# Performance work log

Measured on AMD Instinct MI355X. Metric: run time of the kernel, lower is better.

The kernel has to match this reference:

```python
import jax, jax.numpy as jnp
import numpy as np

EPS = 1e-06
K = 16  # instance ids 1..K
W_IOU, W_VAR, W_SEED = 1.0, 10.0, 1.0


def _lovasz_hinge_flat(logits, labels):
    # logits, labels: (N,) flat; labels in {0,1}
    signs = 2.0 * labels - 1.0
    errors = 1.0 - logits * signs
    perm = jnp.argsort(-errors)  # descending
    errors_sorted = errors[perm]
    gt_sorted = labels[perm]
    gts = gt_sorted.sum()
    intersection = gts - jnp.cumsum(gt_sorted)
    union = gts + jnp.cumsum(1.0 - gt_sorted)
    jaccard = 1.0 - intersection / jnp.maximum(union, 1e-08)
    jaccard = jnp.concatenate([jaccard[:1], jaccard[1:] - jaccard[:-1]])
    return jnp.dot(jax.nn.relu(errors_sorted), jaccard)


def _forward(y_pred, y_true):
    B, C, H, W = y_pred.shape
    D = 2
    off = y_pred[:, :D]              # (B,D,H,W)
    sig = y_pred[:, D:2 * D]         # (B,D,H,W)
    seed = y_pred[:, 2 * D]          # (B,H,W)
    dt = y_pred.dtype

    gy, gx = jnp.meshgrid(jnp.arange(H, dtype=dt), jnp.arange(W, dtype=dt), indexing='ij')
    grid = jnp.stack([gy, gx])       # (D,H,W)
    emb = grid[None] + off           # (B,D,H,W)

    ids = jnp.arange(1, K + 1)
    mask = (y_true[:, None] == ids[None, :, None, None]).astype(dt)  # (B,K,H,W)
    count = mask.sum((2, 3))                                         # (B,K)
    safe = jnp.maximum(count, 1.0)
    present = (count > 0).astype(dt)
    n_present = jnp.maximum(present.sum(), 1.0)

    # per-instance embedding centers
    Ck = jnp.einsum('bkhw,bdhw->bkd', mask, emb) / safe[..., None]   # (B,K,D)
    sb = jnp.maximum(sig, EPS)                                       # (B,D,H,W)
    diff = emb[:, None] - Ck[..., None, None]                        # (B,K,D,H,W)
    quad = diff * diff / (2.0 * sb[:, None] ** 2)
    phi = jnp.clip(jnp.exp(-quad.sum(2)), EPS, 1.0 - EPS)            # (B,K,H,W)
    logits = jnp.log(phi) - jnp.log1p(-phi)

    lov = jax.vmap(_lovasz_hinge_flat)(logits.reshape(B * K, -1), mask.reshape(B * K, -1))
    L_iou = (lov * present.reshape(-1)).sum() / n_present

    # sigma smoothness: mean over instances of mean_{d,pixels in mask}|sig - mean_k(sig)|
    mean_sig = jnp.einsum('bkhw,bdhw->bkd', mask, sig) / safe[..., None]  # (B,K,D)
    dev = (jnp.abs(sig[:, None] - mean_sig[..., None, None]) * mask[:, :, None]).sum((2, 3, 4))
    dev = dev / (D * safe)                                           # (B,K)
    L_var = (dev * present).sum() / n_present

    seed_target = (phi * mask).sum(1)                                # (B,H,W)
    L_seed = jnp.mean((seed - seed_target) ** 2)

    return W_IOU * L_iou + W_VAR * L_var + W_SEED * L_seed


def setup_inputs() -> dict:
    key = jax.random.key(0)
    k1, k2 = jax.random.split(key)
    B, H, W = 4, 768, 768
    y_pred = jax.random.uniform(k1, (B, 5, H, W), dtype=jnp.float32)
    y_true = jax.random.randint(k2, (B, H, W), 0, K + 1)
    return {"y_pred": y_pred, "y_true": y_true}


def reference(y_pred, y_true):
    return _forward(y_pred, y_true)
```

## Files before the change

### kernel.cpp

```cpp
#include <hip/hip_runtime.h>

#define HWPIX 589824
#define Wdim 768
#define Bdim 4
#define Kdim 16
#define NBINS 2048
#define RANGE_F 16.0f
#define BIN_W (RANGE_F / NBINS)
#define INV_BIN_W (NBINS / RANGE_F)
#define EPSf 1e-6f
#define QCLIP 13.8155106f

#define Q4 (HWPIX / 4)
#define NSB 192
#define NBLK (NSB * Bdim)
#define GPI (NSB * 256)

#define ACC_OFF 0
#define LOVARR_OFF 724
#define HIST_OFF_F 1024
#define NHIST (Bdim * Kdim * 2 * NBINS)
#define SPART_OFF (HIST_OFF_F + NHIST + 64)
#define MPART_OFF (SPART_OFF + NBLK * 80)

__global__ __launch_bounds__(256, 3) void k_stats(const float* __restrict__ yp,
                                                  const int* __restrict__ yt,
                                                  float* __restrict__ ws,
                                                  unsigned* __restrict__ hist) {
    int b = blockIdx.y;
    int lane = threadIdx.x & 63;
    int wv = threadIdx.x >> 6;
    __shared__ float lpart[4][80];

    {
        int gtid = (b * NSB + blockIdx.x) * 256 + threadIdx.x;
        for (int i = gtid; i < NHIST + 64; i += NBLK * 256) hist[i] = 0u;
    }

    const float4* bp4 = (const float4*)(yp + (size_t)b * 5 * HWPIX);
    const int4* bt4 = (const int4*)(yt + (size_t)b * HWPIX);

    float acc[80];
#pragma unroll
    for (int v = 0; v < 80; ++v) acc[v] = 0.f;

    for (int p = 0; p < 3; ++p) {
        int g = p * GPI + blockIdx.x * 256 + threadIdx.x;
        float4 voy = bp4[g];
        float4 vox = bp4[g + Q4];
        float4 vsy = bp4[g + 2 * Q4];
        float4 vsx = bp4[g + 3 * Q4];
        int4 vt = bt4[g];
        int hwb = g * 4;
        float oy[4] = {voy.x, voy.y, voy.z, voy.w};
        float ox[4] = {vox.x, vox.y, vox.z, vox.w};
        float sy[4] = {vsy.x, vsy.y, vsy.z, vsy.w};
        float sx[4] = {vsx.x, vsx.y, vsx.z, vsx.w};
        int tt[4] = {vt.x, vt.y, vt.z, vt.w};
#pragma unroll
        for (int j = 0; j < 4; ++j) {
            int hw = hwb + j;
            int h = hw / Wdim;
            int w = hw - h * Wdim;
            int own = tt[j] - 1;
            float vy = (float)h + oy[j];
            float vx = (float)w + ox[j];
#pragma unroll
            for (int k = 0; k < Kdim; ++k) {
                float m = (own == k) ? 1.0f : 0.0f;
                acc[k * 5 + 0] += m;
                acc[k * 5 + 1] = fmaf(m, vy, acc[k * 5 + 1]);
                acc[k * 5 + 2] = fmaf(m, vx, acc[k * 5 + 2]);
                acc[k * 5 + 3] = fmaf(m, sy[j], acc[k * 5 + 3]);
                acc[k * 5 + 4] = fmaf(m, sx[j], acc[k * 5 + 4]);
            }
        }
    }

    bool lo = (lane < 32);
#pragma unroll
    for (int v = 0; v < 40; ++v) {
        float send = lo ? acc[v + 40] : acc[v];
        float got = __shfl_xor(send, 32);
        acc[v] += lo ? got : 0.f;
        acc[v + 40] += lo ? 0.f : got;
    }
#pragma unroll
    for (int v = 0; v < 40; ++v) {
        float x = lo ? acc[v] : acc[v + 40];
#pragma unroll
        for (int o = 16; o >= 1; o >>= 1) x += __shfl_xor(x, o);
        if ((lane & 31) == 0) lpart[wv][lo ? v : v + 40] = x;
    }
    __syncthreads();
    if (threadIdx.x < 80) {
        float v = lpart[0][threadIdx.x] + lpart[1][threadIdx.x] +
                  lpart[2][threadIdx.x] + lpart[3][threadIdx.x];
        ws[SPART_OFF + (size_t)(b * NSB + blockIdx.x) * 80 + threadIdx.x] = v;
    }
}

__global__ void k_centers2(float* __restrict__ ws) {
    int wv = threadIdx.x >> 6;
    int lane = threadIdx.x & 63;
    int gw = blockIdx.x * 4 + wv;
    int b = gw / 80, idx = gw - b * 80;
    const float* sp = ws + SPART_OFF + (size_t)b * NSB * 80 + idx;
    float x = sp[(size_t)lane * 80] + sp[(size_t)(lane + 64) * 80] +
              sp[(size_t)(lane + 128) * 80];
#pragma unroll
    for (int o = 32; o >= 1; o >>= 1) x += __shfl_xor(x, o);
    if (lane == 0) ws[ACC_OFF + b * 80 + idx] = x;
}

__global__ __launch_bounds__(256, 3) void k_main(const float* __restrict__ yp,
                                                 const int* __restrict__ yt,
                                                 float* __restrict__ ws,
                                                 unsigned* __restrict__ hist) {
    int b = blockIdx.y;
    int lane = threadIdx.x & 63;
    int wv = threadIdx.x >> 6;
    __shared__ float ck_s[32];
    __shared__ float4 msw_s[17];
    __shared__ float part[4][2];
    if (threadIdx.x < 16) {
        int k = threadIdx.x;
        const float* a = ws + ACC_OFF + (size_t)b * 80 + k * 5;
        float cnt = a[0];
        float safe = fmaxf(cnt, 1.0f);
        float inv = 1.0f / safe;
        ck_s[k * 2 + 0] = a[1] * inv;
        ck_s[k * 2 + 1] = a[2] * inv;
        float4 mw;
        mw.x = a[3] * inv;
        mw.y = a[4] * inv;
        mw.z = (cnt > 0.f) ? 0.5f / cnt : 0.f;
        mw.w = 0.f;
        msw_s[k] = mw;
    }
    if (threadIdx.x == 16) msw_s[16] = (float4){0.f, 0.f, 0.f, 0.f};
    __syncthreads();

    float cky[Kdim], ckx[Kdim];
#pragma unroll
    for (int k = 0; k < Kdim; ++k) {
        cky[k] = ck_s[k * 2];
        ckx[k] = ck_s[k * 2 + 1];
    }

    unsigned* hb = hist + (size_t)(b * Kdim) * 2 * NBINS;
    unsigned* posnh = hist + (size_t)NHIST;
    const float4* bp4 = (const float4*)(yp + (size_t)b * 5 * HWPIX);
    const int4* bt4 = (const int4*)(yt + (size_t)b * HWPIX);

    float varsum = 0.f, ssum = 0.f;
    for (int p = 0; p < 3; ++p) {
        int g = p * GPI + blockIdx.x * 256 + threadIdx.x;
        float4 voy = bp4[g];
        float4 vox = bp4[g + Q4];
        float4 vsy = bp4[g + 2 * Q4];
        float4 vsx = bp4[g + 3 * Q4];
        float4 vse = bp4[g + 4 * Q4];
        int4 vt = bt4[g];
        int hwb = g * 4;
        float oy[4] = {voy.x, voy.y, voy.z, voy.w};
        float ox[4] = {vox.x, vox.y, vox.z, vox.w};
        float sya[4] = {vsy.x, vsy.y, vsy.z, vsy.w};
        float sxa[4] = {vsx.x, vsx.y, vsx.z, vsx.w};
        float sea[4] = {vse.x, vse.y, vse.z, vse.w};
        int tt[4] = {vt.x, vt.y, vt.z, vt.w};
#pragma unroll
        for (int j = 0; j < 4; ++j) {
            int hw = hwb + j;
            int h = hw / Wdim;
            int w = hw - h * Wdim;
            int own = tt[j] - 1;
            float sy = sya[j], sx = sxa[j];
            float ey = (float)h + oy[j], ex = (float)w + ox[j];
            float sby = fmaxf(sy, EPSf), sbx = fmaxf(sx, EPSf);
            float iy = 0.5f / (sby * sby), ix = 0.5f / (sbx * sbx);

            unsigned sm = 0;
#pragma unroll
            for (int k = 0; k < Kdim; ++k) {
                float dy = ey - cky[k];
                float dx = ex - ckx[k];
                float q = fmaf(dy * dy, iy, dx * dx * ix);
                if (q < QCLIP) sm |= (1u << k);
            }
            int ow = (own >= 0) ? own : 16;
            float4 mw = msw_s[ow];
            float devv = fabsf(sy - mw.x) + fabsf(sx - mw.y);
            varsum = fmaf(devv, mw.z, varsum);

            float st = (own >= 0) ? EPSf : 0.f;
            while (sm) {
                int k = __ffs(sm) - 1;
                sm &= sm - 1;
                float dy = ey - ck_s[k * 2];
                float dx = ex - ck_s[k * 2 + 1];
                float q = fmaf(dy * dy, iy, dx * dx * ix);
                float phi = expf(-q);
                phi = fminf(fmaxf(phi, EPSf), 1.0f - EPSf);
                float lg = logf(phi) - log1pf(-phi);
                bool isPos = (k == own);
                float e;
                if (isPos) {
                    st = phi;
                    atomicAdd(&posnh[b * Kdim + k], 1u);
                    e = 1.0f - lg;
                } else {
                    e = 1.0f + lg;
                }
                if (e > 0.f) {
                    int bin = (int)(e * INV_BIN_W);
                    if (bin > NBINS - 1) bin = NBINS - 1;
                    atomicAdd(&hb[(k * 2 + (isPos ? 1 : 0)) * NBINS + bin], 1u);
                }
            }
            float dd = sea[j] - st;
            ssum = fmaf(dd, dd, ssum);
        }
    }
#pragma unroll
    for (int o = 32; o >= 1; o >>= 1) {
        varsum += __shfl_xor(varsum, o);
        ssum += __shfl_xor(ssum, o);
    }
    if (lane == 0) {
        part[wv][0] = varsum;
        part[wv][1] = ssum;
    }
    __syncthreads();
    if (threadIdx.x < 2) {
        float v = part[0][threadIdx.x] + part[1][threadIdx.x] +
                  part[2][threadIdx.x] + part[3][threadIdx.x];
        ws[MPART_OFF + (size_t)(b * NSB + blockIdx.x) * 2 + threadIdx.x] = v;
    }
}

__global__ void k_lovasz(float* __restrict__ ws, const unsigned* __restrict__ hist) {
    int i = blockIdx.x;
    int lane = threadIdx.x;
    float P = ws[ACC_OFF + i * 5];
    if (P < 0.5f) {
        if (lane == 0) ws[LOVARR_OFF + i] = 0.f;
        return;
    }
    const unsigned* hn = hist + (size_t)i * 2 * NBINS;
    const unsigned* hp = hn + NBINS;
    const unsigned* posnh = hist + (size_t)NHIST;
    const float C_LO = logf(EPSf) - log1pf(-EPSf);
    const int HOTBIN = (int)((1.0f - C_LO) * INV_BIN_W);
    int deficit = (int)(P + 0.5f) - (int)posnh[i];
    int carry_p = 0, carry_n = 0;
    float Jtop = 0.f;
    float trap = 0.f;
    for (int c = NBINS / 64 - 1; c >= 0; --c) {
        int m = c * 64 + lane;
        int vp = (int)hp[m];
        int vn = (int)hn[m];
        if (m == HOTBIN) vp += deficit;
        for (int o = 1; o < 64; o <<= 1) {
            int tp = __shfl_down(vp, o);
            int tn = __shfl_down(vn, o);
            if (lane + o < 64) { vp += tp; vn += tn; }
        }
        float p_edge = (float)(carry_p + vp);
        float n_edge = (float)(carry_n + vn);
        float J = 1.0f - (P - p_edge) / (P + n_edge);
        float Jn = __shfl_down(J, 1);
        if (lane == 63) Jn = Jtop;
        trap += 0.5f * (J + Jn);
        carry_p += __shfl(vp, 0);
        carry_n += __shfl(vn, 0);
        Jtop = __shfl(J, 0);
    }
    for (int o = 1; o < 64; o <<= 1) {
        float t2 = __shfl_down(trap, o);
        if (lane + o < 64) trap += t2;
    }
    if (lane == 0) ws[LOVARR_OFF + i] = trap * BIN_W;
}

__global__ void k_final(const float* __restrict__ ws, float* __restrict__ out) {
    __shared__ float r0[256], r1[256], r2[256], r3[256];
    int t = threadIdx.x;
    float v = 0.f, s = 0.f, l = 0.f, pr = 0.f;
    for (int j = t; j < NBLK; j += 256) {
        v += ws[MPART_OFF + 2 * j];
        s += ws[MPART_OFF + 2 * j + 1];
    }
    if (t < 64) {
        l = ws[LOVARR_OFF + t];
        pr = (ws[ACC_OFF + t * 5] > 0.f) ? 1.f : 0.f;
    }
    r0[t] = v; r1[t] = s; r2[t] = l; r3[t] = pr;
    __syncthreads();
    for (int o = 128; o > 0; o >>= 1) {
        if (t < o) {
            r0[t] += r0[t + o]; r1[t] += r1[t + o];
            r2[t] += r2[t + o]; r3[t] += r3[t + o];
        }
        __syncthreads();
    }
    if (t == 0) {
        float npres = fmaxf(r3[0], 1.0f);
        out[0] = r2[0] / npres + 10.0f * (r0[0] / npres) +
                 r1[0] / (float)((size_t)Bdim * HWPIX);
    }
}

extern "C" void kernel_launch(void* const* d_in, const int* in_sizes, int n_in,
                              void* d_out, int out_size, void* d_ws, size_t ws_size,
                              hipStream_t stream) {
    const float* yp = (const float*)d_in[0];
    const int* yt = (const int*)d_in[1];
    float* ws = (float*)d_ws;
    unsigned* hist = (unsigned*)((char*)d_ws + HIST_OFF_F * 4);

    dim3 g(NSB, Bdim);
    k_stats<<<g, 256, 0, stream>>>(yp, yt, ws, hist);
    k_centers2<<<80, 256, 0, stream>>>(ws);
    k_main<<<g, 256, 0, stream>>>(yp, yt, ws, hist);
    k_lovasz<<<64, 64, 0, stream>>>(ws, hist);
    k_final<<<1, 256, 0, stream>>>(ws, (float*)d_out);
}
```

Measured before the change: 82.74 us.

## Raise grid to 288 blocks per image, split stats accumulators, preload both tiles

Increases blocks per image from 192 to 288 so each thread handles two float4 tiles instead of three, and raises launch_bounds occupancy from 3 to 4. k_stats now splits its 80-register accumulator into two phases (count/centers, then sigma sums) to cut register pressure. k_main issues all loads for both tiles up front to overlap memory latency. The trade-off is more partials for k_centers2 to reduce, which now uses a loop, and reloading the label tile in the second stats phase.

```diff
diff --git a/kernel.cpp b/kernel.cpp
--- a/kernel.cpp
+++ b/kernel.cpp
@@ -12,7 +12,7 @@
 #define QCLIP 13.8155106f
 
 #define Q4 (HWPIX / 4)
-#define NSB 192
+#define NSB 288
 #define NBLK (NSB * Bdim)
 #define GPI (NSB * 256)
 
@@ -23,7 +23,7 @@
 #define SPART_OFF (HIST_OFF_F + NHIST + 64)
 #define MPART_OFF (SPART_OFF + NBLK * 80)
 
-__global__ __launch_bounds__(256, 3) void k_stats(const float* __restrict__ yp,
+__global__ __launch_bounds__(256, 4) void k_stats(const float* __restrict__ yp,
                                                   const int* __restrict__ yt,
                                                   float* __restrict__ ws,
                                                   unsigned* __restrict__ hist) {
@@ -34,64 +34,118 @@
 
     {
         int gtid = (b * NSB + blockIdx.x) * 256 + threadIdx.x;
-        for (int i = gtid; i < NHIST + 64; i += NBLK * 256) hist[i] = 0u;
+        if (gtid < NHIST + 64) hist[gtid] = 0u;
     }
 
     const float4* bp4 = (const float4*)(yp + (size_t)b * 5 * HWPIX);
     const int4* bt4 = (const int4*)(yt + (size_t)b * HWPIX);
-
-    float acc[80];
-#pragma unroll
-    for (int v = 0; v < 80; ++v) acc[v] = 0.f;
-
-    for (int p = 0; p < 3; ++p) {
-        int g = p * GPI + blockIdx.x * 256 + threadIdx.x;
-        float4 voy = bp4[g];
-        float4 vox = bp4[g + Q4];
-        float4 vsy = bp4[g + 2 * Q4];
-        float4 vsx = bp4[g + 3 * Q4];
-        int4 vt = bt4[g];
-        int hwb = g * 4;
-        float oy[4] = {voy.x, voy.y, voy.z, voy.w};
-        float ox[4] = {vox.x, vox.y, vox.z, vox.w};
-        float sy[4] = {vsy.x, vsy.y, vsy.z, vsy.w};
-        float sx[4] = {vsx.x, vsx.y, vsx.z, vsx.w};
-        int tt[4] = {vt.x, vt.y, vt.z, vt.w};
-#pragma unroll
-        for (int j = 0; j < 4; ++j) {
-            int hw = hwb + j;
-            int h = hw / Wdim;
-            int w = hw - h * Wdim;
-            int own = tt[j] - 1;
-            float vy = (float)h + oy[j];
-            float vx = (float)w + ox[j];
-#pragma unroll
-            for (int k = 0; k < Kdim; ++k) {
-                float m = (own == k) ? 1.0f : 0.0f;
-                acc[k * 5 + 0] += m;
-                acc[k * 5 + 1] = fmaf(m, vy, acc[k * 5 + 1]);
-                acc[k * 5 + 2] = fmaf(m, vx, acc[k * 5 + 2]);
-                acc[k * 5 + 3] = fmaf(m, sy[j], acc[k * 5 + 3]);
-                acc[k * 5 + 4] = fmaf(m, sx[j], acc[k * 5 + 4]);
+    int g0 = blockIdx.x * 256 + threadIdx.x;
+    int g1 = g0 + GPI;
+    bool lo = (lane < 32);
+
+    {
+        float acc[48];
+#pragma unroll
+        for (int v = 0; v < 48; ++v) acc[v] = 0.f;
+
+        float4 aoy = bp4[g0], aox = bp4[g0 + Q4];
+        int4 at = bt4[g0];
+        float4 boy = bp4[g1], box = bp4[g1 + Q4];
+        int4 bt = bt4[g1];
+
+#define S1_TILE(voy, vox, vt, gbase)                                          \
+        do {                                                                  \
+            int hwb = (gbase) * 4;                                            \
+            float oy[4] = {voy.x, voy.y, voy.z, voy.w};                       \
+            float ox[4] = {vox.x, vox.y, vox.z, vox.w};                       \
+            int tt[4] = {vt.x, vt.y, vt.z, vt.w};                             \
+            _Pragma("unroll") for (int j = 0; j < 4; ++j) {                   \
+                int hw = hwb + j;                                             \
+                int h = hw / Wdim;                                            \
+                int w = hw - h * Wdim;                                        \
+                int own = tt[j] - 1;                                          \
+                float vy = (float)h + oy[j];                                  \
+                float vx = (float)w + ox[j];                                  \
+                _Pragma("unroll") for (int k = 0; k < Kdim; ++k) {            \
+                    float m = (own == k) ? 1.0f : 0.0f;                       \
+                    acc[k * 3 + 0] += m;                                      \
+                    acc[k * 3 + 1] = fmaf(m, vy, acc[k * 3 + 1]);             \
+                    acc[k * 3 + 2] = fmaf(m, vx, acc[k * 3 + 2]);             \
+                }                                                             \
+            }                                                                 \
+        } while (0)
+
+        S1_TILE(aoy, aox, at, g0);
+        S1_TILE(boy, box, bt, g1);
+#undef S1_TILE
+
+#pragma unroll
+        for (int v = 0; v < 24; ++v) {
+            float send = lo ? acc[v + 24] : acc[v];
+            float got = __shfl_xor(send, 32);
+            acc[v] += lo ? got : 0.f;
+            acc[v + 24] += lo ? 0.f : got;
+        }
+#pragma unroll
+        for (int v = 0; v < 24; ++v) {
+            float x = lo ? acc[v] : acc[v + 24];
+#pragma unroll
+            for (int o = 16; o >= 1; o >>= 1) x += __shfl_xor(x, o);
+            if ((lane & 31) == 0) {
+                int vv = lo ? v : v + 24;
+                lpart[wv][(vv / 3) * 5 + vv % 3] = x;
             }
         }
     }
 
-    bool lo = (lane < 32);
-#pragma unroll
-    for (int v = 0; v < 40; ++v) {
-        float send = lo ? acc[v + 40] : acc[v];
-        float got = __shfl_xor(send, 32);
-        acc[v] += lo ? got : 0.f;
-        acc[v + 40] += lo ? 0.f : got;
-    }
-#pragma unroll
-    for (int v = 0; v < 40; ++v) {
-        float x = lo ? acc[v] : acc[v + 40];
-#pragma unroll
-        for (int o = 16; o >= 1; o >>= 1) x += __shfl_xor(x, o);
-        if ((lane & 31) == 0) lpart[wv][lo ? v : v + 40] = x;
-    }
+    {
+        float acc[32];
+#pragma unroll
+        for (int v = 0; v < 32; ++v) acc[v] = 0.f;
+
+        float4 asy = bp4[g0 + 2 * Q4], asx = bp4[g0 + 3 * Q4];
+        int4 at = bt4[g0];
+        float4 bsy = bp4[g1 + 2 * Q4], bsx = bp4[g1 + 3 * Q4];
+        int4 bt = bt4[g1];
+
+#define S2_TILE(vsy, vsx, vt)                                                 \
+        do {                                                                  \
+            float sy[4] = {vsy.x, vsy.y, vsy.z, vsy.w};                       \
+            float sx[4] = {vsx.x, vsx.y, vsx.z, vsx.w};                       \
+            int tt[4] = {vt.x, vt.y, vt.z, vt.w};                             \
+            _Pragma("unroll") for (int j = 0; j < 4; ++j) {                   \
+                int own = tt[j] - 1;                                          \
+                _Pragma("unroll") for (int k = 0; k < Kdim; ++k) {            \
+                    float m = (own == k) ? 1.0f : 0.0f;                       \
+                    acc[k * 2 + 0] = fmaf(m, sy[j], acc[k * 2 + 0]);          \
+                    acc[k * 2 + 1] = fmaf(m, sx[j], acc[k * 2 + 1]);          \
+                }                                                             \
+            }                                                                 \
+        } while (0)
+
+        S2_TILE(asy, asx, at);
+        S2_TILE(bsy, bsx, bt);
+#undef S2_TILE
+
+#pragma unroll
+        for (int v = 0; v < 16; ++v) {
+            float send = lo ? acc[v + 16] : acc[v];
+            float got = __shfl_xor(send, 32);
+            acc[v] += lo ? got : 0.f;
+            acc[v + 16] += lo ? 0.f : got;
+        }
+#pragma unroll
+        for (int v = 0; v < 16; ++v) {
+            float x = lo ? acc[v] : acc[v + 16];
+#pragma unroll
+            for (int o = 16; o >= 1; o >>= 1) x += __shfl_xor(x, o);
+            if ((lane & 31) == 0) {
+                int vv = lo ? v : v + 16;
+                lpart[wv][(vv / 2) * 5 + 3 + (vv & 1)] = x;
+            }
+        }
+    }
+
     __syncthreads();
     if (threadIdx.x < 80) {
         float v = lpart[0][threadIdx.x] + lpart[1][threadIdx.x] +
@@ -106,14 +160,14 @@
     int gw = blockIdx.x * 4 + wv;
     int b = gw / 80, idx = gw - b * 80;
     const float* sp = ws + SPART_OFF + (size_t)b * NSB * 80 + idx;
-    float x = sp[(size_t)lane * 80] + sp[(size_t)(lane + 64) * 80] +
-              sp[(size_t)(lane + 128) * 80];
+    float x = 0.f;
+    for (int j = lane; j < NSB; j += 64) x += sp[(size_t)j * 80];
 #pragma unroll
     for (int o = 32; o >= 1; o >>= 1) x += __shfl_xor(x, o);
     if (lane == 0) ws[ACC_OFF + b * 80 + idx] = x;
 }
 
-__global__ __launch_bounds__(256, 3) void k_main(const float* __restrict__ yp,
+__global__ __launch_bounds__(256, 4) void k_main(const float* __restrict__ yp,
                                                  const int* __restrict__ yt,
                                                  float* __restrict__ ws,
                                                  unsigned* __restrict__ hist) {
@@ -152,76 +206,81 @@
     unsigned* posnh = hist + (size_t)NHIST;
     const float4* bp4 = (const float4*)(yp + (size_t)b * 5 * HWPIX);
     const int4* bt4 = (const int4*)(yt + (size_t)b * HWPIX);
+    int g0 = blockIdx.x * 256 + threadIdx.x;
+    int g1 = g0 + GPI;
+
+    float4 aoy = bp4[g0], aox = bp4[g0 + Q4], asy = bp4[g0 + 2 * Q4];
+    float4 asx = bp4[g0 + 3 * Q4], ase = bp4[g0 + 4 * Q4];
+    int4 at = bt4[g0];
+    float4 boy = bp4[g1], box = bp4[g1 + Q4], bsy = bp4[g1 + 2 * Q4];
+    float4 bsx = bp4[g1 + 3 * Q4], bse = bp4[g1 + 4 * Q4];
+    int4 btt = bt4[g1];
 
     float varsum = 0.f, ssum = 0.f;
-    for (int p = 0; p < 3; ++p) {
-        int g = p * GPI + blockIdx.x * 256 + threadIdx.x;
-        float4 voy = bp4[g];
-        float4 vox = bp4[g + Q4];
-        float4 vsy = bp4[g + 2 * Q4];
-        float4 vsx = bp4[g + 3 * Q4];
-        float4 vse = bp4[g + 4 * Q4];
-        int4 vt = bt4[g];
-        int hwb = g * 4;
-        float oy[4] = {voy.x, voy.y, voy.z, voy.w};
-        float ox[4] = {vox.x, vox.y, vox.z, vox.w};
-        float sya[4] = {vsy.x, vsy.y, vsy.z, vsy.w};
-        float sxa[4] = {vsx.x, vsx.y, vsx.z, vsx.w};
-        float sea[4] = {vse.x, vse.y, vse.z, vse.w};
-        int tt[4] = {vt.x, vt.y, vt.z, vt.w};
-#pragma unroll
-        for (int j = 0; j < 4; ++j) {
-            int hw = hwb + j;
-            int h = hw / Wdim;
-            int w = hw - h * Wdim;
-            int own = tt[j] - 1;
-            float sy = sya[j], sx = sxa[j];
-            float ey = (float)h + oy[j], ex = (float)w + ox[j];
-            float sby = fmaxf(sy, EPSf), sbx = fmaxf(sx, EPSf);
-            float iy = 0.5f / (sby * sby), ix = 0.5f / (sbx * sbx);
-
-            unsigned sm = 0;
-#pragma unroll
-            for (int k = 0; k < Kdim; ++k) {
-                float dy = ey - cky[k];
-                float dx = ex - ckx[k];
-                float q = fmaf(dy * dy, iy, dx * dx * ix);
-                if (q < QCLIP) sm |= (1u << k);
-            }
-            int ow = (own >= 0) ? own : 16;
-            float4 mw = msw_s[ow];
-            float devv = fabsf(sy - mw.x) + fabsf(sx - mw.y);
-            varsum = fmaf(devv, mw.z, varsum);
-
-            float st = (own >= 0) ? EPSf : 0.f;
-            while (sm) {
-                int k = __ffs(sm) - 1;
-                sm &= sm - 1;
-                float dy = ey - ck_s[k * 2];
-                float dx = ex - ck_s[k * 2 + 1];
-                float q = fmaf(dy * dy, iy, dx * dx * ix);
-                float phi = expf(-q);
-                phi = fminf(fmaxf(phi, EPSf), 1.0f - EPSf);
-                float lg = logf(phi) - log1pf(-phi);
-                bool isPos = (k == own);
-                float e;
-                if (isPos) {
-                    st = phi;
-                    atomicAdd(&posnh[b * Kdim + k], 1u);
-                    e = 1.0f - lg;
-                } else {
-                    e = 1.0f + lg;
-                }
-                if (e > 0.f) {
-                    int bin = (int)(e * INV_BIN_W);
-                    if (bin > NBINS - 1) bin = NBINS - 1;
-                    atomicAdd(&hb[(k * 2 + (isPos ? 1 : 0)) * NBINS + bin], 1u);
-                }
-            }
-            float dd = sea[j] - st;
-            ssum = fmaf(dd, dd, ssum);
-        }
-    }
+
+#define M_TILE(voy, vox, vsy, vsx, vse, vt, gbase)                            \
+    do {                                                                      \
+        int hwb = (gbase) * 4;                                                \
+        float oy[4] = {voy.x, voy.y, voy.z, voy.w};                           \
+        float ox[4] = {vox.x, vox.y, vox.z, vox.w};                           \
+        float sya[4] = {vsy.x, vsy.y, vsy.z, vsy.w};                          \
+        float sxa[4] = {vsx.x, vsx.y, vsx.z, vsx.w};                          \
+        float sea[4] = {vse.x, vse.y, vse.z, vse.w};                          \
+        int tt[4] = {vt.x, vt.y, vt.z, vt.w};                                 \
+        _Pragma("unroll") for (int j = 0; j < 4; ++j) {                       \
+            int hw = hwb + j;                                                 \
+            int h = hw / Wdim;                                                \
+            int w = hw - h * Wdim;                                            \
+            int own = tt[j] - 1;                                              \
+            float sy = sya[j], sx = sxa[j];                                   \
+            float ey = (float)h + oy[j], ex = (float)w + ox[j];               \
+            float sby = fmaxf(sy, EPSf), sbx = fmaxf(sx, EPSf);               \
+            float iy = 0.5f / (sby * sby), ix = 0.5f / (sbx * sbx);           \
+            unsigned sm = 0;                                                  \
+            _Pragma("unroll") for (int k = 0; k < Kdim; ++k) {                \
+                float dy = ey - cky[k];                                       \
+                float dx = ex - ckx[k];                                       \
+                float q = fmaf(dy * dy, iy, dx * dx * ix);                    \
+                if (q < QCLIP) sm |= (1u << k);                               \
+            }                                                                 \
+            int ow = (own >= 0) ? own : 16;                                   \
+            float4 mw = msw_s[ow];                                            \
+            float devv = fabsf(sy - mw.x) + fabsf(sx - mw.y);                 \
+            varsum = fmaf(devv, mw.z, varsum);                                \
+            float st = (own >= 0) ? EPSf : 0.f;                               \
+            while (sm) {                                                      \
+                int k = __ffs(sm) - 1;                                        \
+                sm &= sm - 1;                                                 \
+                float dy = ey - ck_s[k * 2];                                  \
+                float dx = ex - ck_s[k * 2 + 1];                              \
+                float q = fmaf(dy * dy, iy, dx * dx * ix);                    \
+                float phi = expf(-q);                                         \
+                phi = fminf(fmaxf(phi, EPSf), 1.0f - EPSf);                   \
+                float lg = logf(phi) - log1pf(-phi);                          \
+                bool isPos = (k == own);                                      \
+                float e;                                                      \
+                if (isPos) {                                                  \
+                    st = phi;                                                 \
+                    atomicAdd(&posnh[b * Kdim + k], 1u);                      \
+                    e = 1.0f - lg;                                            \
+                } else {                                                      \
+                    e = 1.0f + lg;                                            \
+                }                                                             \
+                if (e > 0.f) {                                                \
+                    int bin = (int)(e * INV_BIN_W);                           \
+                    if (bin > NBINS - 1) bin = NBINS - 1;                     \
+                    atomicAdd(&hb[(k * 2 + (isPos ? 1 : 0)) * NBINS + bin], 1u); \
+                }                                                             \
+            }                                                                 \
+            float dd = sea[j] - st;                                           \
+            ssum = fmaf(dd, dd, ssum);                                        \
+        }                                                                     \
+    } while (0)
+
+    M_TILE(aoy, aox, asy, asx, ase, at, g0);
+    M_TILE(boy, box, bsy, bsx, bse, btt, g1);
+#undef M_TILE
+
 #pragma unroll
     for (int o = 32; o >= 1; o >>= 1) {
         varsum += __shfl_xor(varsum, o);
```

New measurement: 286.9 us. 3.47x slower.

## Split stats kernel into embedding and sigma passes, widen grid, preload tiles

Applied to the files above, without the earlier changes.

The per-instance stats kernel is split into two kernels, one accumulating counts and embedding sums and one accumulating sigma sums, which cuts per-thread accumulator registers from 80 to 48 and 32. The grid grows from 192 to 288 blocks per batch so each thread handles two float4 groups instead of three. All global loads are issued up front before compute, and launch bounds raise the occupancy target to 4 blocks per CU. The cost is an extra kernel launch, a second read of the label array, and a hist zeroing that now relies on the larger grid covering the whole buffer in one pass.

```diff
diff --git a/kernel.cpp b/kernel.cpp
--- a/kernel.cpp
+++ b/kernel.cpp
@@ -12,7 +12,7 @@
 #define QCLIP 13.8155106f
 
 #define Q4 (HWPIX / 4)
-#define NSB 192
+#define NSB 288
 #define NBLK (NSB * Bdim)
 #define GPI (NSB * 256)
 
@@ -23,40 +23,40 @@
 #define SPART_OFF (HIST_OFF_F + NHIST + 64)
 #define MPART_OFF (SPART_OFF + NBLK * 80)
 
-__global__ __launch_bounds__(256, 3) void k_stats(const float* __restrict__ yp,
-                                                  const int* __restrict__ yt,
-                                                  float* __restrict__ ws,
-                                                  unsigned* __restrict__ hist) {
+__global__ __launch_bounds__(256, 4) void k_statsE(const float* __restrict__ yp,
+                                                   const int* __restrict__ yt,
+                                                   float* __restrict__ ws,
+                                                   unsigned* __restrict__ hist) {
     int b = blockIdx.y;
     int lane = threadIdx.x & 63;
     int wv = threadIdx.x >> 6;
-    __shared__ float lpart[4][80];
+    __shared__ float lpart[4][48];
 
     {
         int gtid = (b * NSB + blockIdx.x) * 256 + threadIdx.x;
-        for (int i = gtid; i < NHIST + 64; i += NBLK * 256) hist[i] = 0u;
+        if (gtid < NHIST + 64) hist[gtid] = 0u;
     }
 
     const float4* bp4 = (const float4*)(yp + (size_t)b * 5 * HWPIX);
     const int4* bt4 = (const int4*)(yt + (size_t)b * HWPIX);
-
-    float acc[80];
-#pragma unroll
-    for (int v = 0; v < 80; ++v) acc[v] = 0.f;
-
-    for (int p = 0; p < 3; ++p) {
-        int g = p * GPI + blockIdx.x * 256 + threadIdx.x;
-        float4 voy = bp4[g];
-        float4 vox = bp4[g + Q4];
-        float4 vsy = bp4[g + 2 * Q4];
-        float4 vsx = bp4[g + 3 * Q4];
-        int4 vt = bt4[g];
-        int hwb = g * 4;
+    int g0 = blockIdx.x * 256 + threadIdx.x;
+    int g1 = g0 + GPI;
+
+    float4 aoy = bp4[g0], aox = bp4[g0 + Q4];
+    int4 ait = bt4[g0];
+    float4 boy = bp4[g1], box = bp4[g1 + Q4];
+    int4 bit = bt4[g1];
+
+    float acc[48];
+#pragma unroll
+    for (int v = 0; v < 48; ++v) acc[v] = 0.f;
+
+    auto tile = [&](const float4& voy, const float4& vox, const int4& vt,
+                    int gbase) {
         float oy[4] = {voy.x, voy.y, voy.z, voy.w};
         float ox[4] = {vox.x, vox.y, vox.z, vox.w};
-        float sy[4] = {vsy.x, vsy.y, vsy.z, vsy.w};
-        float sx[4] = {vsx.x, vsx.y, vsx.z, vsx.w};
         int tt[4] = {vt.x, vt.y, vt.z, vt.w};
+        int hwb = gbase * 4;
 #pragma unroll
         for (int j = 0; j < 4; ++j) {
             int hw = hwb + j;
@@ -68,35 +68,100 @@
 #pragma unroll
             for (int k = 0; k < Kdim; ++k) {
                 float m = (own == k) ? 1.0f : 0.0f;
-                acc[k * 5 + 0] += m;
-                acc[k * 5 + 1] = fmaf(m, vy, acc[k * 5 + 1]);
-                acc[k * 5 + 2] = fmaf(m, vx, acc[k * 5 + 2]);
-                acc[k * 5 + 3] = fmaf(m, sy[j], acc[k * 5 + 3]);
-                acc[k * 5 + 4] = fmaf(m, sx[j], acc[k * 5 + 4]);
+                acc[k * 3 + 0] += m;
+                acc[k * 3 + 1] = fmaf(m, vy, acc[k * 3 + 1]);
+                acc[k * 3 + 2] = fmaf(m, vx, acc[k * 3 + 2]);
             }
         }
-    }
+    };
+    tile(aoy, aox, ait, g0);
+    tile(boy, box, bit, g1);
 
     bool lo = (lane < 32);
 #pragma unroll
-    for (int v = 0; v < 40; ++v) {
-        float send = lo ? acc[v + 40] : acc[v];
+    for (int v = 0; v < 24; ++v) {
+        float send = lo ? acc[v + 24] : acc[v];
         float got = __shfl_xor(send, 32);
         acc[v] += lo ? got : 0.f;
-        acc[v + 40] += lo ? 0.f : got;
-    }
-#pragma unroll
-    for (int v = 0; v < 40; ++v) {
-        float x = lo ? acc[v] : acc[v + 40];
+        acc[v + 24] += lo ? 0.f : got;
+    }
+#pragma unroll
+    for (int v = 0; v < 24; ++v) {
+        float x = lo ? acc[v] : acc[v + 24];
 #pragma unroll
         for (int o = 16; o >= 1; o >>= 1) x += __shfl_xor(x, o);
-        if ((lane & 31) == 0) lpart[wv][lo ? v : v + 40] = x;
+        if ((lane & 31) == 0) lpart[wv][lo ? v : v + 24] = x;
     }
     __syncthreads();
-    if (threadIdx.x < 80) {
+    if (threadIdx.x < 48) {
         float v = lpart[0][threadIdx.x] + lpart[1][threadIdx.x] +
                   lpart[2][threadIdx.x] + lpart[3][threadIdx.x];
-        ws[SPART_OFF + (size_t)(b * NSB + blockIdx.x) * 80 + threadIdx.x] = v;
+        int slot = (threadIdx.x / 3) * 5 + threadIdx.x % 3;
+        ws[SPART_OFF + (size_t)(b * NSB + blockIdx.x) * 80 + slot] = v;
+    }
+}
+
+__global__ __launch_bounds__(256, 4) void k_statsS(const float* __restrict__ yp,
+                                                   const int* __restrict__ yt,
+                                                   float* __restrict__ ws) {
+    int b = blockIdx.y;
+    int lane = threadIdx.x & 63;
+    int wv = threadIdx.x >> 6;
+    __shared__ float lpart[4][32];
+
+    const float4* bp4 = (const float4*)(yp + (size_t)b * 5 * HWPIX);
+    const int4* bt4 = (const int4*)(yt + (size_t)b * HWPIX);
+    int g0 = blockIdx.x * 256 + threadIdx.x;
+    int g1 = g0 + GPI;
+
+    float4 asy = bp4[g0 + 2 * Q4], asx = bp4[g0 + 3 * Q4];
+    int4 ait = bt4[g0];
+    float4 bsy = bp4[g1 + 2 * Q4], bsx = bp4[g1 + 3 * Q4];
+    int4 bit = bt4[g1];
+
+    float acc[32];
+#pragma unroll
+    for (int v = 0; v < 32; ++v) acc[v] = 0.f;
+
+    auto tile = [&](const float4& vsy, const float4& vsx, const int4& vt) {
+        float sy[4] = {vsy.x, vsy.y, vsy.z, vsy.w};
+        float sx[4] = {vsx.x, vsx.y, vsx.z, vsx.w};
+        int tt[4] = {vt.x, vt.y, vt.z, vt.w};
+#pragma unroll
+        for (int j = 0; j < 4; ++j) {
+            int own = tt[j] - 1;
+#pragma unroll
+            for (int k = 0; k < Kdim; ++k) {
+                float m = (own == k) ? 1.0f : 0.0f;
+                acc[k * 2 + 0] = fmaf(m, sy[j], acc[k * 2 + 0]);
+                acc[k * 2 + 1] = fmaf(m, sx[j], acc[k * 2 + 1]);
+            }
+        }
+    };
+    tile(asy, asx, ait);
+    tile(bsy, bsx, bit);
+
+    bool lo = (lane < 32);
+#pragma unroll
+    for (int v = 0; v < 16; ++v) {
+        float send = lo ? acc[v + 16] : acc[v];
+        float got = __shfl_xor(send, 32);
+        acc[v] += lo ? got : 0.f;
+        acc[v + 16] += lo ? 0.f : got;
+    }
+#pragma unroll
+    for (int v = 0; v < 16; ++v) {
+        float x = lo ? acc[v] : acc[v + 16];
+#pragma unroll
+        for (int o = 16; o >= 1; o >>= 1) x += __shfl_xor(x, o);
+        if ((lane & 31) == 0) lpart[wv][lo ? v : v + 16] = x;
+    }
+    __syncthreads();
+    if (threadIdx.x < 32) {
+        float v = lpart[0][threadIdx.x] + lpart[1][threadIdx.x] +
+                  lpart[2][threadIdx.x] + lpart[3][threadIdx.x];
+        int slot = (threadIdx.x / 2) * 5 + 3 + (threadIdx.x & 1);
+        ws[SPART_OFF + (size_t)(b * NSB + blockIdx.x) * 80 + slot] = v;
     }
 }
 
@@ -106,14 +171,14 @@
     int gw = blockIdx.x * 4 + wv;
     int b = gw / 80, idx = gw - b * 80;
     const float* sp = ws + SPART_OFF + (size_t)b * NSB * 80 + idx;
-    float x = sp[(size_t)lane * 80] + sp[(size_t)(lane + 64) * 80] +
-              sp[(size_t)(lane + 128) * 80];
+    float x = 0.f;
+    for (int j = lane; j < NSB; j += 64) x += sp[(size_t)j * 80];
 #pragma unroll
     for (int o = 32; o >= 1; o >>= 1) x += __shfl_xor(x, o);
     if (lane == 0) ws[ACC_OFF + b * 80 + idx] = x;
 }
 
-__global__ __launch_bounds__(256, 3) void k_main(const float* __restrict__ yp,
+__global__ __launch_bounds__(256, 4) void k_main(const float* __restrict__ yp,
                                                  const int* __restrict__ yt,
                                                  float* __restrict__ ws,
                                                  unsigned* __restrict__ hist) {
@@ -152,23 +217,28 @@
     unsigned* posnh = hist + (size_t)NHIST;
     const float4* bp4 = (const float4*)(yp + (size_t)b * 5 * HWPIX);
     const int4* bt4 = (const int4*)(yt + (size_t)b * HWPIX);
+    int g0 = blockIdx.x * 256 + threadIdx.x;
+    int g1 = g0 + GPI;
+
+    float4 aoy = bp4[g0], aox = bp4[g0 + Q4], asy = bp4[g0 + 2 * Q4];
+    float4 asx = bp4[g0 + 3 * Q4], ase = bp4[g0 + 4 * Q4];
+    int4 ait = bt4[g0];
+    float4 boy = bp4[g1], box = bp4[g1 + Q4], bsy = bp4[g1 + 2 * Q4];
+    float4 bsx = bp4[g1 + 3 * Q4], bse = bp4[g1 + 4 * Q4];
+    int4 bit = bt4[g1];
 
     float varsum = 0.f, ssum = 0.f;
-    for (int p = 0; p < 3; ++p) {
-        int g = p * GPI + blockIdx.x * 256 + threadIdx.x;
-        float4 voy = bp4[g];
-        float4 vox = bp4[g + Q4];
-        float4 vsy = bp4[g + 2 * Q4];
-        float4 vsx = bp4[g + 3 * Q4];
-        float4 vse = bp4[g + 4 * Q4];
-        int4 vt = bt4[g];
-        int hwb = g * 4;
+
+    auto tile = [&](const float4& voy, const float4& vox, const float4& vsy,
+                    const float4& vsx, const float4& vse, const int4& vt,
+                    int gbase) {
         float oy[4] = {voy.x, voy.y, voy.z, voy.w};
         float ox[4] = {vox.x, vox.y, vox.z, vox.w};
         float sya[4] = {vsy.x, vsy.y, vsy.z, vsy.w};
         float sxa[4] = {vsx.x, vsx.y, vsx.z, vsx.w};
         float sea[4] = {vse.x, vse.y, vse.z, vse.w};
         int tt[4] = {vt.x, vt.y, vt.z, vt.w};
+        int hwb = gbase * 4;
 #pragma unroll
         for (int j = 0; j < 4; ++j) {
             int hw = hwb + j;
@@ -221,7 +291,10 @@
             float dd = sea[j] - st;
             ssum = fmaf(dd, dd, ssum);
         }
-    }
+    };
+    tile(aoy, aox, asy, asx, ase, ait, g0);
+    tile(boy, box, bsy, bsx, bse, bit, g1);
+
 #pragma unroll
     for (int o = 32; o >= 1; o >>= 1) {
         varsum += __shfl_xor(varsum, o);
@@ -320,7 +393,8 @@
     unsigned* hist = (unsigned*)((char*)d_ws + HIST_OFF_F * 4);
 
     dim3 g(NSB, Bdim);
-    k_stats<<<g, 256, 0, stream>>>(yp, yt, ws, hist);
+    k_statsE<<<g, 256, 0, stream>>>(yp, yt, ws, hist);
+    k_statsS<<<g, 256, 0, stream>>>(yp, yt, ws);
     k_centers2<<<80, 256, 0, stream>>>(ws);
     k_main<<<g, 256, 0, stream>>>(yp, yt, ws, hist);
     k_lovasz<<<64, 64, 0, stream>>>(ws, hist);
```

New measurement: 117.1 us. 1.42x slower.

## Prefetch next pixel group in stats/main loops and fuse final reduction into lovasz

Applied to the files above, without the earlier changes.

Both pixel-streaming kernels now load the next group's float4 inputs before computing on the current group, a software-pipelined double buffer meant to hide global memory latency. The separate k_final launch is removed. The last k_lovasz block, chosen by an atomic ticket counter placed in the zeroed histogram tail, performs the final reduction, which saves one kernel launch. The risks are higher register pressure under launch_bounds(256,3) and reliance on threadfence ordering for the last-block pattern.

```diff
diff --git a/kernel.cpp b/kernel.cpp
--- a/kernel.cpp
+++ b/kernel.cpp
@@ -20,7 +20,8 @@
 #define LOVARR_OFF 724
 #define HIST_OFF_F 1024
 #define NHIST (Bdim * Kdim * 2 * NBINS)
-#define SPART_OFF (HIST_OFF_F + NHIST + 64)
+#define HTAIL 80
+#define SPART_OFF (HIST_OFF_F + NHIST + 128)
 #define MPART_OFF (SPART_OFF + NBLK * 80)
 
 __global__ __launch_bounds__(256, 3) void k_stats(const float* __restrict__ yp,
@@ -34,7 +35,7 @@
 
     {
         int gtid = (b * NSB + blockIdx.x) * 256 + threadIdx.x;
-        for (int i = gtid; i < NHIST + 64; i += NBLK * 256) hist[i] = 0u;
+        for (int i = gtid; i < NHIST + HTAIL; i += NBLK * 256) hist[i] = 0u;
     }
 
     const float4* bp4 = (const float4*)(yp + (size_t)b * 5 * HWPIX);
@@ -44,36 +45,52 @@
 #pragma unroll
     for (int v = 0; v < 80; ++v) acc[v] = 0.f;
 
+    int g = blockIdx.x * 256 + threadIdx.x;
+    float4 coy = bp4[g], cox = bp4[g + Q4];
+    float4 csy = bp4[g + 2 * Q4], csx = bp4[g + 3 * Q4];
+    int4 ct = bt4[g];
+
+#pragma unroll
     for (int p = 0; p < 3; ++p) {
-        int g = p * GPI + blockIdx.x * 256 + threadIdx.x;
-        float4 voy = bp4[g];
-        float4 vox = bp4[g + Q4];
-        float4 vsy = bp4[g + 2 * Q4];
-        float4 vsx = bp4[g + 3 * Q4];
-        int4 vt = bt4[g];
-        int hwb = g * 4;
-        float oy[4] = {voy.x, voy.y, voy.z, voy.w};
-        float ox[4] = {vox.x, vox.y, vox.z, vox.w};
-        float sy[4] = {vsy.x, vsy.y, vsy.z, vsy.w};
-        float sx[4] = {vsx.x, vsx.y, vsx.z, vsx.w};
-        int tt[4] = {vt.x, vt.y, vt.z, vt.w};
-#pragma unroll
-        for (int j = 0; j < 4; ++j) {
-            int hw = hwb + j;
-            int h = hw / Wdim;
-            int w = hw - h * Wdim;
-            int own = tt[j] - 1;
-            float vy = (float)h + oy[j];
-            float vx = (float)w + ox[j];
-#pragma unroll
-            for (int k = 0; k < Kdim; ++k) {
-                float m = (own == k) ? 1.0f : 0.0f;
-                acc[k * 5 + 0] += m;
-                acc[k * 5 + 1] = fmaf(m, vy, acc[k * 5 + 1]);
-                acc[k * 5 + 2] = fmaf(m, vx, acc[k * 5 + 2]);
-                acc[k * 5 + 3] = fmaf(m, sy[j], acc[k * 5 + 3]);
-                acc[k * 5 + 4] = fmaf(m, sx[j], acc[k * 5 + 4]);
+        float4 noy, nox, nsy, nsx;
+        int4 nt_;
+        if (p < 2) {
+            int gn = g + GPI;
+            noy = bp4[gn];
+            nox = bp4[gn + Q4];
+            nsy = bp4[gn + 2 * Q4];
+            nsx = bp4[gn + 3 * Q4];
+            nt_ = bt4[gn];
+        }
+        {
+            int hwb = g * 4;
+            float oy[4] = {coy.x, coy.y, coy.z, coy.w};
+            float ox[4] = {cox.x, cox.y, cox.z, cox.w};
+            float sy[4] = {csy.x, csy.y, csy.z, csy.w};
+            float sx[4] = {csx.x, csx.y, csx.z, csx.w};
+            int tt[4] = {ct.x, ct.y, ct.z, ct.w};
+#pragma unroll
+            for (int j = 0; j < 4; ++j) {
+                int hw = hwb + j;
+                int h = hw / Wdim;
+                int w = hw - h * Wdim;
+                int own = tt[j] - 1;
+                float vy = (float)h + oy[j];
+                float vx = (float)w + ox[j];
+#pragma unroll
+                for (int k = 0; k < Kdim; ++k) {
+                    float m = (own == k) ? 1.0f : 0.0f;
+                    acc[k * 5 + 0] += m;
+                    acc[k * 5 + 1] = fmaf(m, vy, acc[k * 5 + 1]);
+                    acc[k * 5 + 2] = fmaf(m, vx, acc[k * 5 + 2]);
+                    acc[k * 5 + 3] = fmaf(m, sy[j], acc[k * 5 + 3]);
+                    acc[k * 5 + 4] = fmaf(m, sx[j], acc[k * 5 + 4]);
+                }
             }
+        }
+        if (p < 2) {
+            coy = noy; cox = nox; csy = nsy; csx = nsx; ct = nt_;
+            g += GPI;
         }
     }
 
@@ -154,74 +171,92 @@
     const int4* bt4 = (const int4*)(yt + (size_t)b * HWPIX);
 
     float varsum = 0.f, ssum = 0.f;
+    int g = blockIdx.x * 256 + threadIdx.x;
+    float4 coy = bp4[g], cox = bp4[g + Q4];
+    float4 csy = bp4[g + 2 * Q4], csx = bp4[g + 3 * Q4];
+    float4 cse = bp4[g + 4 * Q4];
+    int4 ct = bt4[g];
+
+#pragma unroll
     for (int p = 0; p < 3; ++p) {
-        int g = p * GPI + blockIdx.x * 256 + threadIdx.x;
-        float4 voy = bp4[g];
-        float4 vox = bp4[g + Q4];
-        float4 vsy = bp4[g + 2 * Q4];
-        float4 vsx = bp4[g + 3 * Q4];
-        float4 vse = bp4[g + 4 * Q4];
-        int4 vt = bt4[g];
-        int hwb = g * 4;
-        float oy[4] = {voy.x, voy.y, voy.z, voy.w};
-        float ox[4] = {vox.x, vox.y, vox.z, vox.w};
-        float sya[4] = {vsy.x, vsy.y, vsy.z, vsy.w};
-        float sxa[4] = {vsx.x, vsx.y, vsx.z, vsx.w};
-        float sea[4] = {vse.x, vse.y, vse.z, vse.w};
-        int tt[4] = {vt.x, vt.y, vt.z, vt.w};
-#pragma unroll
-        for (int j = 0; j < 4; ++j) {
-            int hw = hwb + j;
-            int h = hw / Wdim;
-            int w = hw - h * Wdim;
-            int own = tt[j] - 1;
-            float sy = sya[j], sx = sxa[j];
-            float ey = (float)h + oy[j], ex = (float)w + ox[j];
-            float sby = fmaxf(sy, EPSf), sbx = fmaxf(sx, EPSf);
-            float iy = 0.5f / (sby * sby), ix = 0.5f / (sbx * sbx);
-
-            unsigned sm = 0;
-#pragma unroll
-            for (int k = 0; k < Kdim; ++k) {
-                float dy = ey - cky[k];
-                float dx = ex - ckx[k];
-                float q = fmaf(dy * dy, iy, dx * dx * ix);
-                if (q < QCLIP) sm |= (1u << k);
+        float4 noy, nox, nsy, nsx, nse;
+        int4 nt_;
+        if (p < 2) {
+            int gn = g + GPI;
+            noy = bp4[gn];
+            nox = bp4[gn + Q4];
+            nsy = bp4[gn + 2 * Q4];
+            nsx = bp4[gn + 3 * Q4];
+            nse = bp4[gn + 4 * Q4];
+            nt_ = bt4[gn];
+        }
+        {
+            int hwb = g * 4;
+            float oy[4] = {coy.x, coy.y, coy.z, coy.w};
+            float ox[4] = {cox.x, cox.y, cox.z, cox.w};
+            float sya[4] = {csy.x, csy.y, csy.z, csy.w};
+            float sxa[4] = {csx.x, csx.y, csx.z, csx.w};
+            float sea[4] = {cse.x, cse.y, cse.z, cse.w};
+            int tt[4] = {ct.x, ct.y, ct.z, ct.w};
+#pragma unroll
+            for (int j = 0; j < 4; ++j) {
+                int hw = hwb + j;
+                int h = hw / Wdim;
+                int w = hw - h * Wdim;
+                int own = tt[j] - 1;
+                float sy = sya[j], sx = sxa[j];
+                float ey = (float)h + oy[j], ex = (float)w + ox[j];
+                float sby = fmaxf(sy, EPSf), sbx = fmaxf(sx, EPSf);
+                float iy = 0.5f / (sby * sby), ix = 0.5f / (sbx * sbx);
+
+                unsigned sm = 0;
+#pragma unroll
+                for (int k = 0; k < Kdim; ++k) {
+                    float dy = ey - cky[k];
+                    float dx = ex - ckx[k];
+                    float q = fmaf(dy * dy, iy, dx * dx * ix);
+                    if (q < QCLIP) sm |= (1u << k);
+                }
+                int ow = (own >= 0) ? own : 16;
+                float4 mw = msw_s[ow];
+                float devv = fabsf(sy - mw.x) + fabsf(sx - mw.y);
+                varsum = fmaf(devv, mw.z, varsum);
+
+                float st = (own >= 0) ? EPSf : 0.f;
+                while (sm) {
+                    int k = __ffs(sm) - 1;
+                    sm &= sm - 1;
+                    float dy = ey - ck_s[k * 2];
+                    float dx = ex - ck_s[k * 2 + 1];
+                    float q = fmaf(dy * dy, iy, dx * dx * ix);
+                    float phi = expf(-q);
+                    phi = fminf(fmaxf(phi, EPSf), 1.0f - EPSf);
+                    float lg = logf(phi) - log1pf(-phi);
+                    bool isPos = (k == own);
+                    float e;
+                    if (isPos) {
+                        st = phi;
+                        atomicAdd(&posnh[b * Kdim + k], 1u);
+                        e = 1.0f - lg;
+                    } else {
+                        e = 1.0f + lg;
+                    }
+                    if (e > 0.f) {
+                        int bin = (int)(e * INV_BIN_W);
+                        if (bin > NBINS - 1) bin = NBINS - 1;
+                        atomicAdd(&hb[(k * 2 + (isPos ? 1 : 0)) * NBINS + bin], 1u);
+                    }
+                }
+                float dd = sea[j] - st;
+                ssum = fmaf(dd, dd, ssum);
             }
-            int ow = (own >= 0) ? own : 16;
-            float4 mw = msw_s[ow];
-            float devv = fabsf(sy - mw.x) + fabsf(sx - mw.y);
-            varsum = fmaf(devv, mw.z, varsum);
-
-            float st = (own >= 0) ? EPSf : 0.f;
-            while (sm) {
-                int k = __ffs(sm) - 1;
-                sm &= sm - 1;
-                float dy = ey - ck_s[k * 2];
-                float dx = ex - ck_s[k * 2 + 1];
-                float q = fmaf(dy * dy, iy, dx * dx * ix);
-                float phi = expf(-q);
-                phi = fminf(fmaxf(phi, EPSf), 1.0f - EPSf);
-                float lg = logf(phi) - log1pf(-phi);
-                bool isPos = (k == own);
-                float e;
-                if (isPos) {
-                    st = phi;
-                    atomicAdd(&posnh[b * Kdim + k], 1u);
-                    e = 1.0f - lg;
-                } else {
-                    e = 1.0f + lg;
-                }
-                if (e > 0.f) {
-                    int bin = (int)(e * INV_BIN_W);
-                    if (bin > NBINS - 1) bin = NBINS - 1;
-                    atomicAdd(&hb[(k * 2 + (isPos ? 1 : 0)) * NBINS + bin], 1u);
-                }
-            }
-            float dd = sea[j] - st;
-            ssum = fmaf(dd, dd, ssum);
-        }
-    }
+        }
+        if (p < 2) {
+            coy = noy; cox = nox; csy = nsy; csx = nsx; cse = nse; ct = nt_;
+            g += GPI;
+        }
+    }
+
 #pragma unroll
     for (int o = 32; o >= 1; o >>= 1) {
         varsum += __shfl_xor(varsum, o);
@@ -239,75 +274,74 @@
     }
 }
 
-__global__ void k_lovasz(float* __restrict__ ws, const unsigned* __restrict__ hist) {
+__global__ void k_lovasz(float* __restrict__ ws, unsigned* __restrict__ hist,
+                         float* __restrict__ out) {
     int i = blockIdx.x;
     int lane = threadIdx.x;
     float P = ws[ACC_OFF + i * 5];
-    if (P < 0.5f) {
-        if (lane == 0) ws[LOVARR_OFF + i] = 0.f;
-        return;
-    }
-    const unsigned* hn = hist + (size_t)i * 2 * NBINS;
-    const unsigned* hp = hn + NBINS;
-    const unsigned* posnh = hist + (size_t)NHIST;
-    const float C_LO = logf(EPSf) - log1pf(-EPSf);
-    const int HOTBIN = (int)((1.0f - C_LO) * INV_BIN_W);
-    int deficit = (int)(P + 0.5f) - (int)posnh[i];
-    int carry_p = 0, carry_n = 0;
-    float Jtop = 0.f;
-    float trap = 0.f;
-    for (int c = NBINS / 64 - 1; c >= 0; --c) {
-        int m = c * 64 + lane;
-        int vp = (int)hp[m];
-        int vn = (int)hn[m];
-        if (m == HOTBIN) vp += deficit;
+    float res = 0.f;
+    if (P >= 0.5f) {
+        const unsigned* hn = hist + (size_t)i * 2 * NBINS;
+        const unsigned* hp = hn + NBINS;
+        const unsigned* posnh = hist + (size_t)NHIST;
+        const float C_LO = logf(EPSf) - log1pf(-EPSf);
+        const int HOTBIN = (int)((1.0f - C_LO) * INV_BIN_W);
+        int deficit = (int)(P + 0.5f) - (int)posnh[i];
+        int carry_p = 0, carry_n = 0;
+        float Jtop = 0.f;
+        float trap = 0.f;
+        for (int c = NBINS / 64 - 1; c >= 0; --c) {
+            int m = c * 64 + lane;
+            int vp = (int)hp[m];
+            int vn = (int)hn[m];
+            if (m == HOTBIN) vp += deficit;
+            for (int o = 1; o < 64; o <<= 1) {
+                int tp = __shfl_down(vp, o);
+                int tn = __shfl_down(vn, o);
+                if (lane + o < 64) { vp += tp; vn += tn; }
+            }
+            float p_edge = (float)(carry_p + vp);
+            float n_edge = (float)(carry_n + vn);
+            float J = 1.0f - (P - p_edge) / (P + n_edge);
+            float Jn = __shfl_down(J, 1);
+            if (lane == 63) Jn = Jtop;
+            trap += 0.5f * (J + Jn);
+            carry_p += __shfl(vp, 0);
+            carry_n += __shfl(vn, 0);
+            Jtop = __shfl(J, 0);
+        }
         for (int o = 1; o < 64; o <<= 1) {
-            int tp = __shfl_down(vp, o);
-            int tn = __shfl_down(vn, o);
-            if (lane + o < 64) { vp += tp; vn += tn; }
-        }
-        float p_edge = (float)(carry_p + vp);
-        float n_edge = (float)(carry_n + vn);
-        float J = 1.0f - (P - p_edge) / (P + n_edge);
-        float Jn = __shfl_down(J, 1);
-        if (lane == 63) Jn = Jtop;
-        trap += 0.5f * (J + Jn);
-        carry_p += __shfl(vp, 0);
-        carry_n += __shfl(vn, 0);
-        Jtop = __shfl(J, 0);
-    }
-    for (int o = 1; o < 64; o <<= 1) {
-        float t2 = __shfl_down(trap, o);
-        if (lane + o < 64) trap += t2;
-    }
-    if (lane == 0) ws[LOVARR_OFF + i] = trap * BIN_W;
-}
-
-__global__ void k_final(const float* __restrict__ ws, float* __restrict__ out) {
-    __shared__ float r0[256], r1[256], r2[256], r3[256];
-    int t = threadIdx.x;
+            float t2 = __shfl_down(trap, o);
+            if (lane + o < 64) trap += t2;
+        }
+        res = trap * BIN_W;
+    }
+    if (lane == 0) ws[LOVARR_OFF + i] = res;
+    __threadfence();
+
+    __shared__ unsigned ticket;
+    if (lane == 0) ticket = atomicAdd(&hist[NHIST + 64], 1u);
+    __syncthreads();
+    if (ticket != 63u) return;
+
     float v = 0.f, s = 0.f, l = 0.f, pr = 0.f;
-    for (int j = t; j < NBLK; j += 256) {
+    for (int j = lane; j < NBLK; j += 64) {
         v += ws[MPART_OFF + 2 * j];
         s += ws[MPART_OFF + 2 * j + 1];
     }
-    if (t < 64) {
-        l = ws[LOVARR_OFF + t];
-        pr = (ws[ACC_OFF + t * 5] > 0.f) ? 1.f : 0.f;
-    }
-    r0[t] = v; r1[t] = s; r2[t] = l; r3[t] = pr;
-    __syncthreads();
-    for (int o = 128; o > 0; o >>= 1) {
-        if (t < o) {
-            r0[t] += r0[t + o]; r1[t] += r1[t + o];
-            r2[t] += r2[t + o]; r3[t] += r3[t + o];
-        }
-        __syncthreads();
-    }
-    if (t == 0) {
-        float npres = fmaxf(r3[0], 1.0f);
-        out[0] = r2[0] / npres + 10.0f * (r0[0] / npres) +
-                 r1[0] / (float)((size_t)Bdim * HWPIX);
+    l = ws[LOVARR_OFF + lane];
+    pr = (ws[ACC_OFF + lane * 5] > 0.f) ? 1.f : 0.f;
+#pragma unroll
+    for (int o = 32; o >= 1; o >>= 1) {
+        v += __shfl_xor(v, o);
+        s += __shfl_xor(s, o);
+        l += __shfl_xor(l, o);
+        pr += __shfl_xor(pr, o);
+    }
+    if (lane == 0) {
+        float npres = fmaxf(pr, 1.0f);
+        out[0] = l / npres + 10.0f * (v / npres) +
+                 s / (float)((size_t)Bdim * HWPIX);
     }
 }
 
@@ -323,6 +357,5 @@
     k_stats<<<g, 256, 0, stream>>>(yp, yt, ws, hist);
     k_centers2<<<80, 256, 0, stream>>>(ws);
     k_main<<<g, 256, 0, stream>>>(yp, yt, ws, hist);
-    k_lovasz<<<64, 64, 0, stream>>>(ws, hist);
-    k_final<<<1, 256, 0, stream>>>(ws, (float*)d_out);
-}
+    k_lovasz<<<64, 64, 0, stream>>>(ws, hist, (float*)d_out);
+}
```

Result: slower. 86.18 us (+4.2%).
